# Optimization experiments

Hardware: AMD Instinct MI355X
Metric: run time of the kernel (lower is better)

## Reference

```python
import jax, jax.numpy as jnp
import numpy as np

TIME_LEN = 640
OUTPUT_DIM = 128
NUM_CHANNELS = 4
T_WAV = 1.0 / 16000
LOG_F_MEAN = 5.02654
LOG_F_STD = 0.373288


def setup_inputs() -> dict:
    key = jax.random.key(0)
    k1, k2, k3, k4, k5 = jax.random.split(key, 5)
    S, B, T, D = 8, 64, TIME_LEN, OUTPUT_DIM
    return {
        "x": jax.random.normal(k1, (S, B, T), dtype=jnp.float32),
        "nlf": jax.random.normal(k2, (S, B, 1), dtype=jnp.float32),
        "tau": jax.random.normal(k3, (S, B, 1), dtype=jnp.float32),
        "a": jax.random.normal(k4, (D,), dtype=jnp.float32),
        "phi": jax.random.normal(k5, (D,), dtype=jnp.float32),
    }


def reference(x, nlf, tau, a, phi):
    # x: [S,B,T], nlf/tau: [S,B,1], a/phi: [D]
    D = a.shape[0]
    # harmonic index per output channel: i = k // num_channels
    i_vec = (jnp.arange(D) // NUM_CHANNELS).astype(x.dtype)  # [D]
    # k_T_tensor: sample times [1,T] scaled by t_wav
    k_T = jnp.arange(TIME_LEN, dtype=x.dtype) * T_WAV  # [T]
    # f = exp(nlf * std + mean): [S,B,1]
    f = jnp.exp(nlf * LOG_F_STD + LOG_F_MEAN)
    # t = k_T - tau: [S,B,T]
    t = k_T[None, None, :] - tau
    # deg[s,b,t,d] = i_d * f_sb * t_sbt + phi_d
    deg = i_vec[None, None, None, :] * (f * t)[..., None] + phi
    # W = a * sin(deg); h_sbd = sum_t W * x
    basis = a * jnp.sin(deg)  # [S,B,T,D]
    h_SBD = jnp.einsum("sbtd,sbt->sbd", basis, x)
    return h_SBD
```

## Files before the change

### kernel.cpp

```cpp
#include <hip/hip_runtime.h>

#define TIME_LEN 640
#define OUT_D 128
#define NUM_SB 512

__global__ __launch_bounds__(512) void sinenet_kernel(
    const float* __restrict__ x,
    const float* __restrict__ nlf,
    const float* __restrict__ tau,
    const float* __restrict__ a,
    const float* __restrict__ phi,
    float* __restrict__ out)
{
    constexpr float T_WAV      = 1.0f / 16000.0f;
    constexpr float LOG_F_STD  = 0.373288f;
    constexpr float LOG_F_MEAN = 5.02654f;
    constexpr double INV_2PI_D = 0.15915494309189535;
    constexpr float  INV_2PI_F = 0.15915494309189535f;

    __shared__ float xs[TIME_LEN];
    __shared__ float PQ[2][32];

    const int sb  = blockIdx.x;
    const int tid = threadIdx.x;

    const float* xrow = x + (size_t)sb * TIME_LEN;
    for (int t = tid; t < TIME_LEN; t += 512) xs[t] = xrow[t];

    const float f = expf(fmaf(nlf[sb], LOG_F_STD, LOG_F_MEAN));
    __syncthreads();

    const int i = tid >> 4;
    const int c = tid & 15;

    const float step_rev = (float)i * f * (T_WAV * INV_2PI_F);
    const float base     = step_rev * (float)c;
    const float step16   = step_rev * 16.0f;

    float P = 0.0f, Q = 0.0f;
    #pragma unroll 8
    for (int k = 0; k < TIME_LEN / 16; ++k) {
        const float rev = fmaf((float)k, step16, base);
        const float rs  = __builtin_amdgcn_fractf(rev);
        const float rc  = __builtin_amdgcn_fractf(rs + 0.25f);
        const float sv  = __builtin_amdgcn_sinf(rs);
        const float cv  = __builtin_amdgcn_sinf(rc);
        const float xv  = xs[c + (k << 4)];
        P = fmaf(xv, sv, P);
        Q = fmaf(xv, cv, Q);
    }
    #pragma unroll
    for (int off = 1; off < 16; off <<= 1) {
        P += __shfl_xor(P, off);
        Q += __shfl_xor(Q, off);
    }
    if (c == 0) { PQ[0][i] = P; PQ[1][i] = Q; }
    __syncthreads();

    if (tid < OUT_D) {
        const int d  = tid;
        const int id = d >> 2;
        double psi = ((double)phi[d]
                    - (double)id * (double)f * (double)tau[sb]) * INV_2PI_D;
        psi -= floor(psi);
        const float pr = (float)psi;
        const float sp = __builtin_amdgcn_sinf(pr);
        const float cp = __builtin_amdgcn_sinf(__builtin_amdgcn_fractf(pr + 0.25f));
        out[(size_t)sb * OUT_D + d] = a[d] * fmaf(cp, PQ[0][id], sp * PQ[1][id]);
    }
}

extern "C" void kernel_launch(void* const* d_in, const int* in_sizes, int n_in,
                              void* d_out, int out_size, void* d_ws, size_t ws_size,
                              hipStream_t stream) {
    const float* x   = (const float*)d_in[0];
    const float* nlf = (const float*)d_in[1];
    const float* tau = (const float*)d_in[2];
    const float* a   = (const float*)d_in[3];
    const float* phi = (const float*)d_in[4];
    float* out = (float*)d_out;

    sinenet_kernel<<<dim3(NUM_SB), dim3(512), 0, stream>>>(x, nlf, tau, a, phi, out);
}
```

Baseline: 9.957 us.

## Replace per-sample sine evaluation with angle-addition recurrence and 1024-thread blocks

Each thread now evaluates sin/cos only once at its starting phase and then advances by a fixed angle step using the rotation (angle-addition) recurrence, instead of calling the hardware sine twice per sample. The block size doubles to 1024 threads with 32 lanes per harmonic, so each thread handles 20 samples instead of 40. The phase-offset sines and the a[] load are hoisted ahead of the first barrier to overlap with the x load. Accumulated rounding error in the recurrence could reduce accuracy at high harmonics.

```diff
diff --git a/kernel.cpp b/kernel.cpp
--- a/kernel.cpp
+++ b/kernel.cpp
@@ -4,7 +4,7 @@
 #define OUT_D 128
 #define NUM_SB 512
 
-__global__ __launch_bounds__(512) void sinenet_kernel(
+__global__ __launch_bounds__(1024) void sinenet_kernel(
     const float* __restrict__ x,
     const float* __restrict__ nlf,
     const float* __restrict__ tau,
@@ -25,32 +25,47 @@
     const int tid = threadIdx.x;
 
     const float* xrow = x + (size_t)sb * TIME_LEN;
-    for (int t = tid; t < TIME_LEN; t += 512) xs[t] = xrow[t];
+    if (tid < TIME_LEN) xs[tid] = xrow[tid];
 
     const float f = expf(fmaf(nlf[sb], LOG_F_STD, LOG_F_MEAN));
+
+    const int i = tid >> 5;
+    const int c = tid & 31;
+
+    float sp = 0.f, cp = 0.f, ad = 0.f;
+    if (tid < OUT_D) {
+        const int id = tid >> 2;
+        double psi = ((double)phi[tid]
+                    - (double)id * (double)f * (double)tau[sb]) * INV_2PI_D;
+        psi -= floor(psi);
+        const float pr = (float)psi;
+        sp = __builtin_amdgcn_sinf(pr);
+        cp = __builtin_amdgcn_sinf(__builtin_amdgcn_fractf(pr + 0.25f));
+        ad = a[tid];
+    }
+
+    const float step_rev = (float)i * f * (T_WAV * INV_2PI_F);
+    const float r0   = __builtin_amdgcn_fractf(step_rev * (float)c);
+    const float rd   = __builtin_amdgcn_fractf(step_rev * 32.0f);
+    float sv = __builtin_amdgcn_sinf(r0);
+    float cv = __builtin_amdgcn_sinf(__builtin_amdgcn_fractf(r0 + 0.25f));
+    const float S = __builtin_amdgcn_sinf(rd);
+    const float C = __builtin_amdgcn_sinf(__builtin_amdgcn_fractf(rd + 0.25f));
+
     __syncthreads();
 
-    const int i = tid >> 4;
-    const int c = tid & 15;
-
-    const float step_rev = (float)i * f * (T_WAV * INV_2PI_F);
-    const float base     = step_rev * (float)c;
-    const float step16   = step_rev * 16.0f;
-
     float P = 0.0f, Q = 0.0f;
-    #pragma unroll 8
-    for (int k = 0; k < TIME_LEN / 16; ++k) {
-        const float rev = fmaf((float)k, step16, base);
-        const float rs  = __builtin_amdgcn_fractf(rev);
-        const float rc  = __builtin_amdgcn_fractf(rs + 0.25f);
-        const float sv  = __builtin_amdgcn_sinf(rs);
-        const float cv  = __builtin_amdgcn_sinf(rc);
-        const float xv  = xs[c + (k << 4)];
+    #pragma unroll 4
+    for (int k = 0; k < TIME_LEN / 32; ++k) {
+        const float xv = xs[c + (k << 5)];
         P = fmaf(xv, sv, P);
         Q = fmaf(xv, cv, Q);
+        const float ns = fmaf(sv, C, cv * S);
+        const float nc = fmaf(cv, C, -sv * S);
+        sv = ns; cv = nc;
     }
     #pragma unroll
-    for (int off = 1; off < 16; off <<= 1) {
+    for (int off = 1; off < 32; off <<= 1) {
         P += __shfl_xor(P, off);
         Q += __shfl_xor(Q, off);
     }
@@ -58,15 +73,8 @@
     __syncthreads();
 
     if (tid < OUT_D) {
-        const int d  = tid;
-        const int id = d >> 2;
-        double psi = ((double)phi[d]
-                    - (double)id * (double)f * (double)tau[sb]) * INV_2PI_D;
-        psi -= floor(psi);
-        const float pr = (float)psi;
-        const float sp = __builtin_amdgcn_sinf(pr);
-        const float cp = __builtin_amdgcn_sinf(__builtin_amdgcn_fractf(pr + 0.25f));
-        out[(size_t)sb * OUT_D + d] = a[d] * fmaf(cp, PQ[0][id], sp * PQ[1][id]);
+        const int id = tid >> 2;
+        out[(size_t)sb * OUT_D + tid] = ad * fmaf(cp, PQ[0][id], sp * PQ[1][id]);
     }
 }
 
@@ -80,5 +88,5 @@
     const float* phi = (const float*)d_in[4];
     float* out = (float*)d_out;
 
-    sinenet_kernel<<<dim3(NUM_SB), dim3(512), 0, stream>>>(x, nlf, tau, a, phi, out);
+    sinenet_kernel<<<dim3(NUM_SB), dim3(1024), 0, stream>>>(x, nlf, tau, a, phi, out);
 }
```

Result: faster. 9.725 us (-2.3%).
